# Optimization experiments

Hardware: AMD Instinct MI355X
Metric: run time of the kernel (lower is better)

The kernel has to match this reference:

```python
import jax, jax.numpy as jnp
import numpy as np

B, L = 32, 512
D_EMB = 500      # tagger_mlp_layer
LANG = 100       # tagger_embeddings_size
H = 800          # tagger_encoder_size * 2
P_ARC = 100      # parser_arc_proj_size
P_LAB = 400      # parser_label_proj_size
MLP = 500        # tagger_mlp_layer (aux_mlp out)
N_LANG, N_LAB, N_UPOS, N_XPOS, N_ATTRS = 8, 50, 20, 300, 500


def setup_inputs() -> dict:
    key = jax.random.key(0)
    ks = jax.random.split(key, 24)
    s = 0.05
    lang_table = jax.random.normal(ks[3], (N_LANG, LANG), jnp.float32) * s
    lang_table = lang_table.at[0].set(0.0)  # padding_idx=0
    return {
        "emb": jax.random.normal(ks[0], (B, L, D_EMB), jnp.float32),
        "hidden": jax.random.normal(ks[1], (B, L, H), jnp.float32),
        "lang_ids": jax.random.randint(ks[2], (B,), 0, N_LANG),
        "lang_table": lang_table,
        "W_arc": jax.random.normal(ks[4], (P_ARC, D_EMB + LANG), jnp.float32) * s,
        "b_arc": jax.random.normal(ks[5], (P_ARC,), jnp.float32) * s,
        "W_lab": jax.random.normal(ks[6], (P_LAB, D_EMB + LANG), jnp.float32) * s,
        "b_lab": jax.random.normal(ks[7], (P_LAB,), jnp.float32) * s,
        "w_head": jax.random.normal(ks[8], (2 * P_ARC,), jnp.float32) * s,
        "b_head": jax.random.normal(ks[9], (1,), jnp.float32) * s,
        "W_aux": jax.random.normal(ks[10], (MLP, H), jnp.float32) * s,
        "b_aux": jax.random.normal(ks[11], (MLP,), jnp.float32) * s,
        "W_upos": jax.random.normal(ks[12], (N_UPOS, MLP + LANG), jnp.float32) * s,
        "b_upos": jax.random.normal(ks[13], (N_UPOS,), jnp.float32) * s,
        "W_xpos": jax.random.normal(ks[14], (N_XPOS, MLP + LANG), jnp.float32) * s,
        "b_xpos": jax.random.normal(ks[15], (N_XPOS,), jnp.float32) * s,
        "W_attrs": jax.random.normal(ks[16], (N_ATTRS, MLP + LANG), jnp.float32) * s,
        "b_attrs": jax.random.normal(ks[17], (N_ATTRS,), jnp.float32) * s,
    }


def reference(emb, hidden, lang_ids, lang_table, W_arc, b_arc, W_lab, b_lab,
              w_head, b_head, W_aux, b_aux, W_upos, b_upos, W_xpos, b_xpos,
              W_attrs, b_attrs):
    Bv, Lv = emb.shape[0], emb.shape[1]
    lang_emb = lang_table[lang_ids]                              # [B, LANG]
    lang_rep = jnp.broadcast_to(lang_emb[:, None, :], (Bv, Lv, lang_emb.shape[-1]))
    ho = jnp.concatenate((emb, lang_rep), axis=2)                # [B, L, D_EMB+LANG]

    proj_arc = jnp.tanh(jnp.einsum('bld,pd->blp', ho, W_arc) + b_arc)   # [B, L, P_ARC]
    proj_label = jnp.tanh(jnp.einsum('bld,pd->blp', ho, W_lab) + b_lab) # [B, L, P_LAB]

    # Biaffine decomposition of output_head(cat(pa[i], pa[j])):
    # score(i,j) = pa[i] . w1 + pa[j] . w2 + b
    P = proj_arc.shape[-1]
    s1 = proj_arc @ w_head[:P]                                   # [B, L]
    s2 = proj_arc @ w_head[P:]                                   # [B, L]
    core = s1[:, :, None] + s2[:, None, :] + b_head[0]           # [B, L, L]
    arcs = jnp.concatenate(
        (jnp.zeros((Bv, Lv, 1), core.dtype), core), axis=2)     # [B, L, L+1]

    aux_hid = jnp.tanh(jnp.einsum('blh,mh->blm', hidden, W_aux) + b_aux)  # [B, L, MLP]
    aux_cat = jnp.concatenate((aux_hid, lang_rep), axis=2)
    s_upos = jnp.einsum('blm,um->blu', aux_cat, W_upos) + b_upos
    s_xpos = jnp.einsum('blm,um->blu', aux_cat, W_xpos) + b_xpos
    s_attrs = jnp.einsum('blm,um->blu', aux_cat, W_attrs) + b_attrs
    return arcs, proj_label, s_upos, s_xpos, s_attrs
```

## Files before the change

### kernel.cpp

```cpp
#include <hip/hip_runtime.h>


using f16   = _Float16;
using f16x4 = __attribute__((ext_vector_type(4))) _Float16;
using f16x8 = __attribute__((ext_vector_type(8))) _Float16;
using f32x4 = __attribute__((ext_vector_type(4))) float;

__device__ __forceinline__ f16 f2h(float f) { return (f16)f; }
__device__ __forceinline__ f16x4 cvt4(float4 v) {
  return f16x4{ f2h(v.x), f2h(v.y), f2h(v.z), f2h(v.w) };
}

__device__ __forceinline__ float fast_tanh(float x) {
  float xc = fminf(fmaxf(x, -15.f), 15.f);
  float e  = __builtin_amdgcn_exp2f(xc * 2.885390081777927f);
  return 1.f - 2.f * __builtin_amdgcn_rcpf(e + 1.f);
}

__device__ __forceinline__ void async16(void* lds, const void* gp) {
  __builtin_amdgcn_global_load_lds(
      (const __attribute__((address_space(1))) unsigned int*)gp,
      (__attribute__((address_space(3))) unsigned int*)lds, 16, 0, 0);
}

__global__ __launch_bounds__(256) void setup_kernel(
    const float* __restrict__ emb, const float* __restrict__ hidden,
    const float* __restrict__ lang_table, const int* __restrict__ lang_ids,
    const float* __restrict__ W_arc, const float* __restrict__ b_arc,
    const float* __restrict__ W_lab, const float* __restrict__ b_lab,
    const float* __restrict__ W_aux, const float* __restrict__ b_aux,
    const float* __restrict__ W_upos, const float* __restrict__ b_upos,
    const float* __restrict__ W_xpos, const float* __restrict__ b_xpos,
    const float* __restrict__ W_attrs, const float* __restrict__ b_attrs,
    f16* __restrict__ ho, f16* __restrict__ aux_cat, f16* __restrict__ hid16,
    f16* __restrict__ W_proj, f16* __restrict__ W_auxp, f16* __restrict__ W_heads,
    float* __restrict__ bias_proj, float* __restrict__ bias_aux, float* __restrict__ bias_heads)
{
  const int HID_Q = 16384 * 208;
  const int HO_Q  = 16384 * 160;
  const int W_Q   = 81920 + 106496 + 163840;
  const int TOTAL = HID_Q + HO_Q + W_Q;

  for (int q = blockIdx.x * 256 + threadIdx.x; q < TOTAL; q += gridDim.x * 256) {
    if (q < HID_Q) {
      int row = q / 208, s = q - row * 208;
      f16x4 h = { (f16)0.f, (f16)0.f, (f16)0.f, (f16)0.f };
      if (s < 200) h = cvt4(*(const float4*)(hidden + (size_t)row * 800 + 4 * s));
      *(f16x4*)(hid16 + (size_t)row * 832 + 4 * s) = h;
    } else if (q < HID_Q + HO_Q) {
      int p = q - HID_Q;
      int row = p / 160, s = p - row * 160;
      f16* horow = ho + (size_t)row * 640;
      if (s < 125) {
        float4 v = *(const float4*)(emb + (size_t)row * 500 + 4 * s);
        *(f16x4*)(horow + 4 * s) = cvt4(v);
      } else {
        f16x4 h = { (f16)0.f, (f16)0.f, (f16)0.f, (f16)0.f };
        if (s < 150) {
          const float* lrow = lang_table + (size_t)lang_ids[row >> 9] * 100;
          h = cvt4(*(const float4*)(lrow + (s - 125) * 4));
        }
        *(f16x4*)(horow + 4 * s) = h;
        *(f16x4*)(aux_cat + (size_t)row * 640 + 4 * s) = h;
      }
    } else {
      int w = q - (HID_Q + HO_Q);
      const float* src = nullptr;
      f16* dst;
      if (w < 81920) {
        int n = w / 160, s = w - n * 160;
        dst = W_proj + (size_t)w * 4;
        if (s < 150 && n < 500)
          src = (n < 100 ? W_arc + (size_t)n * 600
                         : W_lab + (size_t)(n - 100) * 600) + s * 4;
      } else if (w < 81920 + 106496) {
        int w2 = w - 81920;
        int n = w2 / 208, s = w2 - n * 208;
        dst = W_auxp + (size_t)w2 * 4;
        if (s < 200 && n < 500) src = W_aux + (size_t)n * 800 + s * 4;
      } else {
        int w3 = w - (81920 + 106496);
        int n = w3 / 160, s = w3 - n * 160;
        dst = W_heads + (size_t)w3 * 4;
        if (s < 150 && n < 820)
          src = (n < 20 ? W_upos + (size_t)n * 600
                : n < 320 ? W_xpos + (size_t)(n - 20) * 600
                          : W_attrs + (size_t)(n - 320) * 600) + s * 4;
      }
      f16x4 h = { (f16)0.f, (f16)0.f, (f16)0.f, (f16)0.f };
      if (src) h = cvt4(*(const float4*)src);
      *(f16x4*)dst = h;
    }
  }

  if (blockIdx.x == 0) {
    for (int idx = threadIdx.x; idx < 2048; idx += 256) {
      if (idx < 512) {
        float v = 0.f;
        if (idx < 100)      v = b_arc[idx];
        else if (idx < 500) v = b_lab[idx - 100];
        bias_proj[idx] = v;
      } else if (idx < 1024) {
        int i = idx - 512;
        bias_aux[i] = (i < 500) ? b_aux[i] : 0.f;
      } else {
        int i = idx - 1024; float v = 0.f;
        if (i < 20)       v = b_upos[i];
        else if (i < 320) v = b_xpos[i - 20];
        else if (i < 820) v = b_attrs[i - 320];
        bias_heads[i] = v;
      }
    }
  }
}

__device__ __forceinline__ void gemm_core256(
    const f16* __restrict__ A, const f16* __restrict__ Bm,
    const int K, const int NT, const int bm, const int bn,
    f16* __restrict__ ldsA, f16* __restrict__ ldsB, f32x4 (&acc)[8][4])
{
  const int tid  = threadIdx.x;
  const int lane = tid & 63;
  const int wave = tid >> 6;
  const int wm = wave >> 2, wn = wave & 3;
  const int m16 = lane & 15, quad = lane >> 4;

  const int sr = lane >> 3;
  const int ss = (lane & 7) ^ sr;
  const f16* gA[4]; const f16* gB[4];
#pragma unroll
  for (int i = 0; i < 4; ++i) {
    gA[i] = A  + (size_t)(bm * 256 + i * 64 + wave * 8 + sr) * K + ss * 8;
    gB[i] = Bm + (size_t)(bn * 256 + i * 64 + wave * 8 + sr) * K + ss * 8;
  }
  f16* sA = ldsA + wave * 512;
  f16* sB = ldsB + wave * 512;

  const int aBase = (wm * 128 + m16) * 64;
  const int bBase = (wn * 64  + m16) * 64;
  const int sw0 = ((quad)     ^ (m16 & 7)) * 8;
  const int sw1 = ((4 | quad) ^ (m16 & 7)) * 8;

  f16x8 af[4], bf[4];

#define RDA(mqv, sw) { _Pragma("unroll")                                        \
  for (int ii = 0; ii < 4; ++ii)                                                \
    af[ii] = *(const f16x8*)&ldsA[buf + aBase + (mqv) * 4096 + ii * 1024 + (sw)]; }
#define RDB(sw) { _Pragma("unroll")                                             \
  for (int j = 0; j < 4; ++j)                                                   \
    bf[j] = *(const f16x8*)&ldsB[buf + bBase + j * 1024 + (sw)]; }
#define MM(mqv) { _Pragma("unroll")                                             \
  for (int ii = 0; ii < 4; ++ii) { _Pragma("unroll")                            \
    for (int j = 0; j < 4; ++j)                                                 \
      acc[(mqv) * 4 + ii][j] = __builtin_amdgcn_mfma_f32_16x16x32_f16(          \
          af[ii], bf[j], acc[(mqv) * 4 + ii][j], 0, 0, 0); } }
#define VM2 { asm volatile("s_waitcnt vmcnt(2)" ::: "memory");                  \
              __builtin_amdgcn_sched_barrier(0); }
#define VM0 { asm volatile("s_waitcnt vmcnt(0)" ::: "memory");                  \
              __builtin_amdgcn_sched_barrier(0); }
#define BAR  __builtin_amdgcn_s_barrier()
#define PRIO1 __builtin_amdgcn_s_setprio(1)
#define PRIO0 __builtin_amdgcn_s_setprio(0)

#pragma unroll
  for (int i = 0; i < 4; ++i) async16(sB + i * 4096, gB[i]);
#pragma unroll
  for (int i = 0; i < 4; ++i) async16(sA + i * 4096, gA[i]);
  VM0;
  BAR;

  for (int t = 0; t < NT; ++t) {
    const int buf = (t & 1) << 14;
    const int nbf = ((t + 1) & 1) << 14;
    const bool st = (t + 1 < NT);
    const int k0n = (t + 1) << 6;

    if (st) { async16(sB + nbf + 0 * 4096, gB[0] + k0n);
              async16(sB + nbf + 1 * 4096, gB[1] + k0n); }
    RDB(sw0); RDA(0, sw0);
    BAR;
    PRIO1; MM(0); PRIO0;
    if (t > 0) { if (st) VM2 else VM0 }
    BAR;
    if (st) { async16(sB + nbf + 2 * 4096, gB[2] + k0n);
              async16(sB + nbf + 3 * 4096, gB[3] + k0n); }
    RDA(1, sw0);
    BAR;
    PRIO1; MM(1); PRIO0;
    BAR;
    if (st) { async16(sA + nbf + 0 * 4096, gA[0] + k0n);
              async16(sA + nbf + 2 * 4096, gA[2] + k0n); }
    RDB(sw1); RDA(0, sw1);
    BAR;
    PRIO1; MM(0); PRIO0;
    BAR;
    if (st) { async16(sA + nbf + 1 * 4096, gA[1] + k0n);
              async16(sA + nbf + 3 * 4096, gA[3] + k0n); }
    RDA(1, sw1);
    BAR;
    PRIO1; MM(1); PRIO0;
    if (st) VM2;
    BAR;
  }
#undef RDA
#undef RDB
#undef MM
#undef VM2
#undef VM0
#undef BAR
#undef PRIO1
#undef PRIO0
}

__global__ __launch_bounds__(512, 2) void gemm01(
    const f16* __restrict__ ho, const f16* __restrict__ hid16,
    const f16* __restrict__ W_proj, const f16* __restrict__ W_auxp,
    const float* __restrict__ bias_proj, const float* __restrict__ bias_aux,
    float* __restrict__ out_label, const float* __restrict__ w_head,
    float* __restrict__ s1, float* __restrict__ s2, f16* __restrict__ aux_cat)
{
  __shared__ __align__(16) f16 ldsA[2 * 16384];
  __shared__ __align__(16) f16 ldsB[2 * 16384];
  __shared__ float s1red[2][256], s2red[2][256];

  const int tid  = threadIdx.x;
  const int lane = tid & 63;
  const int wave = tid >> 6;
  const int wm = wave >> 2, wn = wave & 3;
  const int m16 = lane & 15, quad = lane >> 4;
  const int bm  = blockIdx.x;
  const int bny = blockIdx.y;
  const bool is0 = (bny < 2);
  const int bn  = is0 ? bny : bny - 2;

  const f16* A = is0 ? ho : hid16;
  const f16* B = is0 ? W_proj : W_auxp;
  const float* bias = is0 ? bias_proj : bias_aux;
  const int K  = is0 ? 640 : 832;
  const int NT = is0 ? 10 : 13;

  f32x4 acc[8][4] = {};
  gemm_core256(A, B, K, NT, bm, bn, ldsA, ldsB, acc);

  const int row0 = bm * 256 + wm * 128 + quad * 4;
  const int colT = bn * 256 + wn * 64 + m16;

  if (is0) {
    float p1[8][4] = {}, p2[8][4] = {};
    const bool haveHead = (bn == 0);
#pragma unroll
    for (int ai = 0; ai < 8; ++ai) {
#pragma unroll
      for (int j = 0; j < 4; ++j) {
        const int col = colT + j * 16;
        const float bcol = bias[col];
        float w1c = 0.f, w2c = 0.f;
        if (haveHead && col < 100) { w1c = w_head[col]; w2c = w_head[100 + col]; }
#pragma unroll
        for (int r = 0; r < 4; ++r) {
          const int row = row0 + ai * 16 + r;
          float v = fast_tanh(acc[ai][j][r] + bcol);
          if (col >= 100 && col < 500) out_label[(size_t)row * 400 + col - 100] = v;
          p1[ai][r] += v * w1c;
          p2[ai][r] += v * w2c;
        }
      }
    }
    if (haveHead) {
      if (wn < 2) {
#pragma unroll
        for (int d = 1; d < 16; d <<= 1)
#pragma unroll
          for (int ai = 0; ai < 8; ++ai)
#pragma unroll
            for (int r = 0; r < 4; ++r) {
              p1[ai][r] += __shfl_xor(p1[ai][r], d);
              p2[ai][r] += __shfl_xor(p2[ai][r], d);
            }
        if (m16 == 0) {
#pragma unroll
          for (int ai = 0; ai < 8; ++ai)
#pragma unroll
            for (int r = 0; r < 4; ++r) {
              int rl = wm * 128 + ai * 16 + quad * 4 + r;
              s1red[wn][rl] = p1[ai][r];
              s2red[wn][rl] = p2[ai][r];
            }
        }
      }
      __syncthreads();
      if (tid < 256) s1[bm * 256 + tid] = s1red[0][tid] + s1red[1][tid];
      else { int t2 = tid - 256; s2[bm * 256 + t2] = s2red[0][t2] + s2red[1][t2]; }
    }
  } else {
#pragma unroll
    for (int ai = 0; ai < 8; ++ai)
#pragma unroll
      for (int j = 0; j < 4; ++j) {
        const int col = colT + j * 16;
        if (col < 500) {
          const float bcol = bias[col];
#pragma unroll
          for (int r = 0; r < 4; ++r) {
            const int row = row0 + ai * 16 + r;
            aux_cat[(size_t)row * 640 + col] = f2h(fast_tanh(acc[ai][j][r] + bcol));
          }
        }
      }
  }
}

__global__ __launch_bounds__(512, 2) void gemm2_arcs(
    const f16* __restrict__ aux_cat, const f16* __restrict__ W_heads,
    const float* __restrict__ bias_heads,
    const float* __restrict__ s1, const float* __restrict__ s2,
    const float* __restrict__ b_head,
    float* __restrict__ out_arcs, float* __restrict__ out_upos,
    float* __restrict__ out_xpos, float* __restrict__ out_attrs)
{
  __shared__ __align__(16) f16 ldsA[2 * 16384];
  __shared__ __align__(16) f16 ldsB[2 * 16384];

  const int tid  = threadIdx.x;
  const int lane = tid & 63;
  const int wave = tid >> 6;
  const int wm = wave >> 2, wn = wave & 3;
  const int m16 = lane & 15, quad = lane >> 4;
  const int bm = blockIdx.x, bn = blockIdx.y;

  f32x4 acc[8][4] = {};
  gemm_core256(aux_cat, W_heads, 640, 10, bm, bn, ldsA, ldsB, acc);

  const int row0 = bm * 256 + wm * 128 + quad * 4;
  const int colT = bn * 256 + wn * 64 + m16;
#pragma unroll
  for (int ai = 0; ai < 8; ++ai)
#pragma unroll
    for (int j = 0; j < 4; ++j) {
      const int col = colT + j * 16;
      const float bcol = bias_heads[col];
#pragma unroll
      for (int r = 0; r < 4; ++r) {
        const int row = row0 + ai * 16 + r;
        float v = acc[ai][j][r] + bcol;
        if (col < 20)        out_upos[(size_t)row * 20 + col] = v;
        else if (col < 320)  out_xpos[(size_t)row * 300 + col - 20] = v;
        else if (col < 820)  out_attrs[(size_t)row * 500 + col - 320] = v;
      }
    }

  const int r0 = bm * 256 + bn * 64;
  const float bh = b_head[0];
  const float s2v = s2[((r0 >> 9) << 9) + tid];
  for (int rl = 0; rl < 64; ++rl) {
    const int row = r0 + rl;
    const float s1v = s1[row] + bh;
    float* orow = out_arcs + (size_t)row * 513;
    if (tid == 0) orow[0] = 0.f;
    orow[1 + tid] = s1v + s2v;
  }
}

extern "C" void kernel_launch(void* const* d_in, const int* in_sizes, int n_in,
                              void* d_out, int out_size, void* d_ws, size_t ws_size,
                              hipStream_t stream)
{
  const float* emb      = (const float*)d_in[0];
  const float* hidden   = (const float*)d_in[1];
  const int*   lang_ids = (const int*)d_in[2];
  const float* lang_tab = (const float*)d_in[3];
  const float* W_arc  = (const float*)d_in[4];
  const float* b_arc  = (const float*)d_in[5];
  const float* W_lab  = (const float*)d_in[6];
  const float* b_lab  = (const float*)d_in[7];
  const float* w_head = (const float*)d_in[8];
  const float* b_head = (const float*)d_in[9];
  const float* W_aux  = (const float*)d_in[10];
  const float* b_aux  = (const float*)d_in[11];
  const float* W_upos = (const float*)d_in[12];
  const float* b_upos = (const float*)d_in[13];
  const float* W_xpos = (const float*)d_in[14];
  const float* b_xpos = (const float*)d_in[15];
  const float* W_attrs = (const float*)d_in[16];
  const float* b_attrs = (const float*)d_in[17];

  char* ws = (char*)d_ws;
  f16* ho      = (f16*)(ws + 0);
  f16* aux_cat = (f16*)(ws + 20971520);
  f16* hid16   = (f16*)(ws + 41943040);
  f16* W_proj  = (f16*)(ws + 69206016);
  f16* W_auxp  = (f16*)(ws + 69861376);
  f16* W_heads = (f16*)(ws + 70713344);
  float* bias_proj  = (float*)(ws + 72024064);
  float* bias_aux   = (float*)(ws + 72026112);
  float* bias_heads = (float*)(ws + 72028160);
  float* s1         = (float*)(ws + 72032256);
  float* s2         = (float*)(ws + 72097792);

  float* out       = (float*)d_out;
  float* out_arcs  = out;
  float* out_label = out + 8404992;
  float* out_upos  = out + 14958592;
  float* out_xpos  = out + 15286272;
  float* out_attrs = out + 20201472;

  setup_kernel<<<2048, 256, 0, stream>>>(
      emb, hidden, lang_tab, lang_ids,
      W_arc, b_arc, W_lab, b_lab, W_aux, b_aux,
      W_upos, b_upos, W_xpos, b_xpos, W_attrs, b_attrs,
      ho, aux_cat, hid16, W_proj, W_auxp, W_heads,
      bias_proj, bias_aux, bias_heads);

  gemm01<<<dim3(64, 4), 512, 0, stream>>>(
      ho, hid16, W_proj, W_auxp, bias_proj, bias_aux,
      out_label, w_head, s1, s2, aux_cat);

  gemm2_arcs<<<dim3(64, 4), 512, 0, stream>>>(
      aux_cat, W_heads, bias_heads, s1, s2, b_head,
      out_arcs, out_upos, out_xpos, out_attrs);
}
```

Baseline: 299.0 us.

## Fuse fp32-to-fp16 activation conversion into the first GEMM's A-tile loads

```diff
diff --git a/kernel.cpp b/kernel.cpp
--- a/kernel.cpp
+++ b/kernel.cpp
@@ -24,123 +24,323 @@
 }
 
 __global__ __launch_bounds__(256) void setup_kernel(
-    const float* __restrict__ emb, const float* __restrict__ hidden,
-    const float* __restrict__ lang_table, const int* __restrict__ lang_ids,
     const float* __restrict__ W_arc, const float* __restrict__ b_arc,
     const float* __restrict__ W_lab, const float* __restrict__ b_lab,
     const float* __restrict__ W_aux, const float* __restrict__ b_aux,
     const float* __restrict__ W_upos, const float* __restrict__ b_upos,
     const float* __restrict__ W_xpos, const float* __restrict__ b_xpos,
     const float* __restrict__ W_attrs, const float* __restrict__ b_attrs,
-    f16* __restrict__ ho, f16* __restrict__ aux_cat, f16* __restrict__ hid16,
     f16* __restrict__ W_proj, f16* __restrict__ W_auxp, f16* __restrict__ W_heads,
     float* __restrict__ bias_proj, float* __restrict__ bias_aux, float* __restrict__ bias_heads)
 {
-  const int HID_Q = 16384 * 208;
-  const int HO_Q  = 16384 * 160;
-  const int W_Q   = 81920 + 106496 + 163840;
-  const int TOTAL = HID_Q + HO_Q + W_Q;
-
-  for (int q = blockIdx.x * 256 + threadIdx.x; q < TOTAL; q += gridDim.x * 256) {
-    if (q < HID_Q) {
-      int row = q / 208, s = q - row * 208;
-      f16x4 h = { (f16)0.f, (f16)0.f, (f16)0.f, (f16)0.f };
-      if (s < 200) h = cvt4(*(const float4*)(hidden + (size_t)row * 800 + 4 * s));
-      *(f16x4*)(hid16 + (size_t)row * 832 + 4 * s) = h;
-    } else if (q < HID_Q + HO_Q) {
-      int p = q - HID_Q;
-      int row = p / 160, s = p - row * 160;
-      f16* horow = ho + (size_t)row * 640;
-      if (s < 125) {
-        float4 v = *(const float4*)(emb + (size_t)row * 500 + 4 * s);
-        *(f16x4*)(horow + 4 * s) = cvt4(v);
-      } else {
-        f16x4 h = { (f16)0.f, (f16)0.f, (f16)0.f, (f16)0.f };
-        if (s < 150) {
-          const float* lrow = lang_table + (size_t)lang_ids[row >> 9] * 100;
-          h = cvt4(*(const float4*)(lrow + (s - 125) * 4));
-        }
-        *(f16x4*)(horow + 4 * s) = h;
-        *(f16x4*)(aux_cat + (size_t)row * 640 + 4 * s) = h;
-      }
+  const int blk = blockIdx.x, t = threadIdx.x;
+  if (blk < 1376) {
+    int w = blk * 256 + t;
+    const float* src = nullptr;
+    f16* dst;
+    if (w < 81920) {
+      int n = w / 160, s = w - n * 160;
+      dst = W_proj + (size_t)w * 4;
+      if (s < 150 && n < 500)
+        src = (n < 100 ? W_arc + (size_t)n * 600
+                       : W_lab + (size_t)(n - 100) * 600) + s * 4;
+    } else if (w < 81920 + 106496) {
+      int w2 = w - 81920;
+      int n = w2 / 208, s = w2 - n * 208;
+      dst = W_auxp + (size_t)w2 * 4;
+      if (s < 200 && n < 500) src = W_aux + (size_t)n * 800 + s * 4;
     } else {
-      int w = q - (HID_Q + HO_Q);
-      const float* src = nullptr;
-      f16* dst;
-      if (w < 81920) {
-        int n = w / 160, s = w - n * 160;
-        dst = W_proj + (size_t)w * 4;
-        if (s < 150 && n < 500)
-          src = (n < 100 ? W_arc + (size_t)n * 600
-                         : W_lab + (size_t)(n - 100) * 600) + s * 4;
-      } else if (w < 81920 + 106496) {
-        int w2 = w - 81920;
-        int n = w2 / 208, s = w2 - n * 208;
-        dst = W_auxp + (size_t)w2 * 4;
-        if (s < 200 && n < 500) src = W_aux + (size_t)n * 800 + s * 4;
-      } else {
-        int w3 = w - (81920 + 106496);
-        int n = w3 / 160, s = w3 - n * 160;
-        dst = W_heads + (size_t)w3 * 4;
-        if (s < 150 && n < 820)
-          src = (n < 20 ? W_upos + (size_t)n * 600
-                : n < 320 ? W_xpos + (size_t)(n - 20) * 600
-                          : W_attrs + (size_t)(n - 320) * 600) + s * 4;
-      }
-      f16x4 h = { (f16)0.f, (f16)0.f, (f16)0.f, (f16)0.f };
-      if (src) h = cvt4(*(const float4*)src);
-      *(f16x4*)dst = h;
-    }
-  }
-
-  if (blockIdx.x == 0) {
-    for (int idx = threadIdx.x; idx < 2048; idx += 256) {
-      if (idx < 512) {
-        float v = 0.f;
-        if (idx < 100)      v = b_arc[idx];
-        else if (idx < 500) v = b_lab[idx - 100];
-        bias_proj[idx] = v;
-      } else if (idx < 1024) {
-        int i = idx - 512;
-        bias_aux[i] = (i < 500) ? b_aux[i] : 0.f;
-      } else {
-        int i = idx - 1024; float v = 0.f;
-        if (i < 20)       v = b_upos[i];
-        else if (i < 320) v = b_xpos[i - 20];
-        else if (i < 820) v = b_attrs[i - 320];
-        bias_heads[i] = v;
-      }
-    }
-  }
-}
-
-__device__ __forceinline__ void gemm_core256(
-    const f16* __restrict__ A, const f16* __restrict__ Bm,
-    const int K, const int NT, const int bm, const int bn,
-    f16* __restrict__ ldsA, f16* __restrict__ ldsB, f32x4 (&acc)[8][4])
+      int w3 = w - (81920 + 106496);
+      int n = w3 / 160, s = w3 - n * 160;
+      dst = W_heads + (size_t)w3 * 4;
+      if (s < 150 && n < 820)
+        src = (n < 20 ? W_upos + (size_t)n * 600
+              : n < 320 ? W_xpos + (size_t)(n - 20) * 600
+                        : W_attrs + (size_t)(n - 320) * 600) + s * 4;
+    }
+    f16x4 h = { (f16)0.f, (f16)0.f, (f16)0.f, (f16)0.f };
+    if (src) h = cvt4(*(const float4*)src);
+    *(f16x4*)dst = h;
+    return;
+  }
+  for (int idx = t; idx < 2048; idx += 256) {
+    if (idx < 512) {
+      float v = 0.f;
+      if (idx < 100)      v = b_arc[idx];
+      else if (idx < 500) v = b_lab[idx - 100];
+      bias_proj[idx] = v;
+    } else if (idx < 1024) {
+      int i = idx - 512;
+      bias_aux[i] = (i < 500) ? b_aux[i] : 0.f;
+    } else {
+      int i = idx - 1024; float v = 0.f;
+      if (i < 20)       v = b_upos[i];
+      else if (i < 320) v = b_xpos[i - 20];
+      else if (i < 820) v = b_attrs[i - 320];
+      bias_heads[i] = v;
+    }
+  }
+}
+
+__global__ __launch_bounds__(512, 2) void gemm01(
+    const float* __restrict__ emb, const float* __restrict__ hidden,
+    const float* __restrict__ lang_table, const int* __restrict__ lang_ids,
+    const f16* __restrict__ W_proj, const f16* __restrict__ W_auxp,
+    const float* __restrict__ bias_proj, const float* __restrict__ bias_aux,
+    float* __restrict__ out_label, const float* __restrict__ w_head,
+    float* __restrict__ s1, float* __restrict__ s2, f16* __restrict__ aux_cat)
 {
+  __shared__ __align__(16) f16 ldsA[2 * 16384];
+  __shared__ __align__(16) f16 ldsB[2 * 16384];
+  __shared__ float s1red[2][256], s2red[2][256];
+
   const int tid  = threadIdx.x;
   const int lane = tid & 63;
   const int wave = tid >> 6;
   const int wm = wave >> 2, wn = wave & 3;
   const int m16 = lane & 15, quad = lane >> 4;
+  const int bm  = blockIdx.x;
+  const int bny = blockIdx.y;
+  const bool is0 = (bny < 2);
+  const int bn  = is0 ? bny : bny - 2;
+  const int K   = is0 ? 640 : 832;
+  const int NT  = is0 ? 10 : 13;
 
   const int sr = lane >> 3;
-  const int ss = (lane & 7) ^ sr;
-  const f16* gA[4]; const f16* gB[4];
+  const int ssB = (lane & 7) ^ sr;
+  const f16* Bmat = is0 ? W_proj : W_auxp;
+  const f16* gB[4];
+#pragma unroll
+  for (int i = 0; i < 4; ++i)
+    gB[i] = Bmat + (size_t)(bn * 256 + i * 64 + wave * 8 + sr) * K + ssB * 8;
+  f16* sB = ldsB + wave * 512;
+
+  const int ssA = lane & 7;
+  const float* lrow = lang_table + (size_t)lang_ids[bm >> 1] * 100;
+  const float* srcA[4];
+  int dstA[4];
 #pragma unroll
   for (int i = 0; i < 4; ++i) {
-    gA[i] = A  + (size_t)(bm * 256 + i * 64 + wave * 8 + sr) * K + ss * 8;
-    gB[i] = Bm + (size_t)(bn * 256 + i * 64 + wave * 8 + sr) * K + ss * 8;
-  }
-  f16* sA = ldsA + wave * 512;
-  f16* sB = ldsB + wave * 512;
+    const int rowA = wave * 32 + i * 8 + (lane >> 3);
+    const int grow = bm * 256 + rowA;
+    srcA[i] = is0 ? emb + (size_t)grow * 500 : hidden + (size_t)grow * 800;
+    dstA[i] = rowA * 64 + ((ssA ^ (rowA & 7)) * 8);
+  }
+  float4 va[4], vb[4];
 
   const int aBase = (wm * 128 + m16) * 64;
   const int bBase = (wn * 64  + m16) * 64;
   const int sw0 = ((quad)     ^ (m16 & 7)) * 8;
   const int sw1 = ((4 | quad) ^ (m16 & 7)) * 8;
 
+  f32x4 acc[8][4] = {};
+  f16x8 af[4], bf[4];
+
+#define ASTAGE(tt) do { const int k0b = (tt) * 64 + ssA * 8;                    \
+    _Pragma("unroll")                                                           \
+    for (int i2 = 0; i2 < 4; ++i2) {                                            \
+      float4 x0 = {0.f,0.f,0.f,0.f}, x1 = {0.f,0.f,0.f,0.f};                    \
+      if (is0) {                                                                \
+        if (k0b < 500) { x0 = *(const float4*)(srcA[i2] + k0b);                 \
+          x1 = (k0b + 4 < 500) ? *(const float4*)(srcA[i2] + k0b + 4)           \
+                               : *(const float4*)(lrow); }                      \
+        else if (k0b < 600) { x0 = *(const float4*)(lrow + k0b - 500);          \
+                              x1 = *(const float4*)(lrow + k0b - 496); }        \
+      } else if (k0b < 800) { x0 = *(const float4*)(srcA[i2] + k0b);            \
+                              x1 = *(const float4*)(srcA[i2] + k0b + 4); }      \
+      va[i2] = x0; vb[i2] = x1; } } while (0)
+
+#define AWRITE(nbf) do { _Pragma("unroll")                                      \
+    for (int i2 = 0; i2 < 4; ++i2) {                                            \
+      f16x8 hw = { f2h(va[i2].x), f2h(va[i2].y), f2h(va[i2].z), f2h(va[i2].w),  \
+                   f2h(vb[i2].x), f2h(vb[i2].y), f2h(vb[i2].z), f2h(vb[i2].w) };\
+      *(f16x8*)&ldsA[(nbf) + dstA[i2]] = hw; } } while (0)
+
+#define RDA(mqv, sw) { _Pragma("unroll")                                        \
+  for (int ii = 0; ii < 4; ++ii)                                                \
+    af[ii] = *(const f16x8*)&ldsA[buf + aBase + (mqv) * 4096 + ii * 1024 + (sw)]; }
+#define RDB(sw) { _Pragma("unroll")                                             \
+  for (int j = 0; j < 4; ++j)                                                   \
+    bf[j] = *(const f16x8*)&ldsB[buf + bBase + j * 1024 + (sw)]; }
+#define MM(mqv) { _Pragma("unroll")                                             \
+  for (int ii = 0; ii < 4; ++ii) { _Pragma("unroll")                            \
+    for (int j = 0; j < 4; ++j)                                                 \
+      acc[(mqv) * 4 + ii][j] = __builtin_amdgcn_mfma_f32_16x16x32_f16(          \
+          af[ii], bf[j], acc[(mqv) * 4 + ii][j], 0, 0, 0); } }
+#define VM0 { asm volatile("s_waitcnt vmcnt(0)" ::: "memory");                  \
+              __builtin_amdgcn_sched_barrier(0); }
+#define LGK0 { asm volatile("s_waitcnt lgkmcnt(0)" ::: "memory");               \
+               __builtin_amdgcn_sched_barrier(0); }
+#define BAR  __builtin_amdgcn_s_barrier()
+#define PRIO1 __builtin_amdgcn_s_setprio(1)
+#define PRIO0 __builtin_amdgcn_s_setprio(0)
+
+#pragma unroll
+  for (int i = 0; i < 4; ++i) async16(sB + i * 4096, gB[i]);
+  ASTAGE(0);
+  VM0;
+  AWRITE(0);
+  LGK0;
+  BAR;
+
+  for (int t = 0; t < NT; ++t) {
+    const int buf = (t & 1) << 14;
+    const int nbf = ((t + 1) & 1) << 14;
+    const bool st = (t + 1 < NT);
+    const int k0n = (t + 1) << 6;
+
+    if (st) {
+      async16(sB + nbf + 0 * 4096, gB[0] + k0n);
+      async16(sB + nbf + 1 * 4096, gB[1] + k0n);
+      async16(sB + nbf + 2 * 4096, gB[2] + k0n);
+      async16(sB + nbf + 3 * 4096, gB[3] + k0n);
+      ASTAGE(t + 1);
+    }
+    RDB(sw0); RDA(0, sw0);
+    BAR;
+    PRIO1; MM(0); PRIO0;
+    BAR;
+    RDA(1, sw0);
+    BAR;
+    PRIO1; MM(1); PRIO0;
+    BAR;
+    RDB(sw1); RDA(0, sw1);
+    BAR;
+    PRIO1; MM(0); PRIO0;
+    BAR;
+    RDA(1, sw1);
+    if (st) { VM0; AWRITE(nbf); }
+    LGK0;
+    BAR;
+    PRIO1; MM(1); PRIO0;
+    BAR;
+  }
+#undef ASTAGE
+#undef AWRITE
+#undef RDA
+#undef RDB
+#undef MM
+#undef VM0
+#undef LGK0
+#undef BAR
+#undef PRIO1
+#undef PRIO0
+
+  const int row0 = bm * 256 + wm * 128 + quad * 4;
+  const int colT = bn * 256 + wn * 64 + m16;
+
+  if (is0) {
+    const float* bias = bias_proj;
+    float p1[8][4] = {}, p2[8][4] = {};
+    const bool haveHead = (bn == 0);
+#pragma unroll
+    for (int ai = 0; ai < 8; ++ai) {
+#pragma unroll
+      for (int j = 0; j < 4; ++j) {
+        const int col = colT + j * 16;
+        const float bcol = bias[col];
+        float w1c = 0.f, w2c = 0.f;
+        if (haveHead && col < 100) { w1c = w_head[col]; w2c = w_head[100 + col]; }
+#pragma unroll
+        for (int r = 0; r < 4; ++r) {
+          const int row = row0 + ai * 16 + r;
+          float v = fast_tanh(acc[ai][j][r] + bcol);
+          if (col >= 100 && col < 500) out_label[(size_t)row * 400 + col - 100] = v;
+          p1[ai][r] += v * w1c;
+          p2[ai][r] += v * w2c;
+        }
+      }
+    }
+    if (haveHead) {
+      if (wn < 2) {
+#pragma unroll
+        for (int d = 1; d < 16; d <<= 1)
+#pragma unroll
+          for (int ai = 0; ai < 8; ++ai)
+#pragma unroll
+            for (int r = 0; r < 4; ++r) {
+              p1[ai][r] += __shfl_xor(p1[ai][r], d);
+              p2[ai][r] += __shfl_xor(p2[ai][r], d);
+            }
+        if (m16 == 0) {
+#pragma unroll
+          for (int ai = 0; ai < 8; ++ai)
+#pragma unroll
+            for (int r = 0; r < 4; ++r) {
+              int rl = wm * 128 + ai * 16 + quad * 4 + r;
+              s1red[wn][rl] = p1[ai][r];
+              s2red[wn][rl] = p2[ai][r];
+            }
+        }
+      }
+      __syncthreads();
+      if (tid < 256) s1[bm * 256 + tid] = s1red[0][tid] + s1red[1][tid];
+      else { int t2 = tid - 256; s2[bm * 256 + t2] = s2red[0][t2] + s2red[1][t2]; }
+    }
+  } else {
+    const float* bias = bias_aux;
+#pragma unroll
+    for (int ai = 0; ai < 8; ++ai)
+#pragma unroll
+      for (int j = 0; j < 4; ++j) {
+        const int col = colT + j * 16;
+        if (col < 500) {
+          const float bcol = bias[col];
+#pragma unroll
+          for (int r = 0; r < 4; ++r) {
+            const int row = row0 + ai * 16 + r;
+            aux_cat[(size_t)row * 640 + col] = f2h(fast_tanh(acc[ai][j][r] + bcol));
+          }
+        }
+      }
+    if (bn == 0) {
+      for (int idx = tid; idx < 256 * 35; idx += 512) {
+        int rr = idx / 35, qq = idx - rr * 35;
+        int col = 500 + 4 * qq;
+        f16x4 h = { (f16)0.f, (f16)0.f, (f16)0.f, (f16)0.f };
+        if (col < 600) h = cvt4(*(const float4*)(lrow + col - 500));
+        *(f16x4*)(aux_cat + (size_t)(bm * 256 + rr) * 640 + col) = h;
+      }
+    }
+  }
+}
+
+__global__ __launch_bounds__(512, 2) void gemm2_arcs(
+    const f16* __restrict__ aux_cat, const f16* __restrict__ W_heads,
+    const float* __restrict__ bias_heads,
+    const float* __restrict__ s1, const float* __restrict__ s2,
+    const float* __restrict__ b_head,
+    float* __restrict__ out_arcs, float* __restrict__ out_upos,
+    float* __restrict__ out_xpos, float* __restrict__ out_attrs)
+{
+  __shared__ __align__(16) f16 ldsA[2 * 16384];
+  __shared__ __align__(16) f16 ldsB[2 * 16384];
+
+  const int tid  = threadIdx.x;
+  const int lane = tid & 63;
+  const int wave = tid >> 6;
+  const int wm = wave >> 2, wn = wave & 3;
+  const int m16 = lane & 15, quad = lane >> 4;
+  const int bm = blockIdx.x, bn = blockIdx.y;
+  const int K = 640, NT = 10;
+
+  const int sr = lane >> 3;
+  const int ss = (lane & 7) ^ sr;
+  const f16* gA[4]; const f16* gB[4];
+#pragma unroll
+  for (int i = 0; i < 4; ++i) {
+    gA[i] = aux_cat + (size_t)(bm * 256 + i * 64 + wave * 8 + sr) * K + ss * 8;
+    gB[i] = W_heads + (size_t)(bn * 256 + i * 64 + wave * 8 + sr) * K + ss * 8;
+  }
+  f16* sA = ldsA + wave * 512;
+  f16* sB = ldsB + wave * 512;
+
+  const int aBase = (wm * 128 + m16) * 64;
+  const int bBase = (wn * 64  + m16) * 64;
+  const int sw0 = ((quad)     ^ (m16 & 7)) * 8;
+  const int sw1 = ((4 | quad) ^ (m16 & 7)) * 8;
+
+  f32x4 acc[8][4] = {};
   f16x8 af[4], bf[4];
 
 #define RDA(mqv, sw) { _Pragma("unroll")                                        \
@@ -210,126 +410,6 @@
 #undef BAR
 #undef PRIO1
 #undef PRIO0
-}
-
-__global__ __launch_bounds__(512, 2) void gemm01(
-    const f16* __restrict__ ho, const f16* __restrict__ hid16,
-    const f16* __restrict__ W_proj, const f16* __restrict__ W_auxp,
-    const float* __restrict__ bias_proj, const float* __restrict__ bias_aux,
-    float* __restrict__ out_label, const float* __restrict__ w_head,
-    float* __restrict__ s1, float* __restrict__ s2, f16* __restrict__ aux_cat)
-{
-  __shared__ __align__(16) f16 ldsA[2 * 16384];
-  __shared__ __align__(16) f16 ldsB[2 * 16384];
-  __shared__ float s1red[2][256], s2red[2][256];
-
-  const int tid  = threadIdx.x;
-  const int lane = tid & 63;
-  const int wave = tid >> 6;
-  const int wm = wave >> 2, wn = wave & 3;
-  const int m16 = lane & 15, quad = lane >> 4;
-  const int bm  = blockIdx.x;
-  const int bny = blockIdx.y;
-  const bool is0 = (bny < 2);
-  const int bn  = is0 ? bny : bny - 2;
-
-  const f16* A = is0 ? ho : hid16;
-  const f16* B = is0 ? W_proj : W_auxp;
-  const float* bias = is0 ? bias_proj : bias_aux;
-  const int K  = is0 ? 640 : 832;
-  const int NT = is0 ? 10 : 13;
-
-  f32x4 acc[8][4] = {};
-  gemm_core256(A, B, K, NT, bm, bn, ldsA, ldsB, acc);
-
-  const int row0 = bm * 256 + wm * 128 + quad * 4;
-  const int colT = bn * 256 + wn * 64 + m16;
-
-  if (is0) {
-    float p1[8][4] = {}, p2[8][4] = {};
-    const bool haveHead = (bn == 0);
-#pragma unroll
-    for (int ai = 0; ai < 8; ++ai) {
-#pragma unroll
-      for (int j = 0; j < 4; ++j) {
-        const int col = colT + j * 16;
-        const float bcol = bias[col];
-        float w1c = 0.f, w2c = 0.f;
-        if (haveHead && col < 100) { w1c = w_head[col]; w2c = w_head[100 + col]; }
-#pragma unroll
-        for (int r = 0; r < 4; ++r) {
-          const int row = row0 + ai * 16 + r;
-          float v = fast_tanh(acc[ai][j][r] + bcol);
-          if (col >= 100 && col < 500) out_label[(size_t)row * 400 + col - 100] = v;
-          p1[ai][r] += v * w1c;
-          p2[ai][r] += v * w2c;
-        }
-      }
-    }
-    if (haveHead) {
-      if (wn < 2) {
-#pragma unroll
-        for (int d = 1; d < 16; d <<= 1)
-#pragma unroll
-          for (int ai = 0; ai < 8; ++ai)
-#pragma unroll
-            for (int r = 0; r < 4; ++r) {
-              p1[ai][r] += __shfl_xor(p1[ai][r], d);
-              p2[ai][r] += __shfl_xor(p2[ai][r], d);
-            }
-        if (m16 == 0) {
-#pragma unroll
-          for (int ai = 0; ai < 8; ++ai)
-#pragma unroll
-            for (int r = 0; r < 4; ++r) {
-              int rl = wm * 128 + ai * 16 + quad * 4 + r;
-              s1red[wn][rl] = p1[ai][r];
-              s2red[wn][rl] = p2[ai][r];
-            }
-        }
-      }
-      __syncthreads();
-      if (tid < 256) s1[bm * 256 + tid] = s1red[0][tid] + s1red[1][tid];
-      else { int t2 = tid - 256; s2[bm * 256 + t2] = s2red[0][t2] + s2red[1][t2]; }
-    }
-  } else {
-#pragma unroll
-    for (int ai = 0; ai < 8; ++ai)
-#pragma unroll
-      for (int j = 0; j < 4; ++j) {
-        const int col = colT + j * 16;
-        if (col < 500) {
-          const float bcol = bias[col];
-#pragma unroll
-          for (int r = 0; r < 4; ++r) {
-            const int row = row0 + ai * 16 + r;
-            aux_cat[(size_t)row * 640 + col] = f2h(fast_tanh(acc[ai][j][r] + bcol));
-          }
-        }
-      }
-  }
-}
-
-__global__ __launch_bounds__(512, 2) void gemm2_arcs(
-    const f16* __restrict__ aux_cat, const f16* __restrict__ W_heads,
-    const float* __restrict__ bias_heads,
-    const float* __restrict__ s1, const float* __restrict__ s2,
-    const float* __restrict__ b_head,
-    float* __restrict__ out_arcs, float* __restrict__ out_upos,
-    float* __restrict__ out_xpos, float* __restrict__ out_attrs)
-{
-  __shared__ __align__(16) f16 ldsA[2 * 16384];
-  __shared__ __align__(16) f16 ldsB[2 * 16384];
-
-  const int tid  = threadIdx.x;
-  const int lane = tid & 63;
-  const int wave = tid >> 6;
-  const int wm = wave >> 2, wn = wave & 3;
-  const int m16 = lane & 15, quad = lane >> 4;
-  const int bm = blockIdx.x, bn = blockIdx.y;
-
-  f32x4 acc[8][4] = {};
-  gemm_core256(aux_cat, W_heads, 640, 10, bm, bn, ldsA, ldsB, acc);
 
   const int row0 = bm * 256 + wm * 128 + quad * 4;
   const int colT = bn * 256 + wn * 64 + m16;
@@ -385,17 +465,15 @@
   const float* b_attrs = (const float*)d_in[17];
 
   char* ws = (char*)d_ws;
-  f16* ho      = (f16*)(ws + 0);
-  f16* aux_cat = (f16*)(ws + 20971520);
-  f16* hid16   = (f16*)(ws + 41943040);
-  f16* W_proj  = (f16*)(ws + 69206016);
-  f16* W_auxp  = (f16*)(ws + 69861376);
-  f16* W_heads = (f16*)(ws + 70713344);
-  float* bias_proj  = (float*)(ws + 72024064);
-  float* bias_aux   = (float*)(ws + 72026112);
-  float* bias_heads = (float*)(ws + 72028160);
-  float* s1         = (float*)(ws + 72032256);
-  float* s2         = (float*)(ws + 72097792);
+  f16* aux_cat = (f16*)(ws + 0);
+  f16* W_proj  = (f16*)(ws + 20971520);
+  f16* W_auxp  = (f16*)(ws + 21626880);
+  f16* W_heads = (f16*)(ws + 22478848);
+  float* bias_proj  = (float*)(ws + 23789568);
+  float* bias_aux   = (float*)(ws + 23791616);
+  float* bias_heads = (float*)(ws + 23793664);
+  float* s1         = (float*)(ws + 23797760);
+  float* s2         = (float*)(ws + 23863296);
 
   float* out       = (float*)d_out;
   float* out_arcs  = out;
@@ -404,15 +482,13 @@
   float* out_xpos  = out + 15286272;
   float* out_attrs = out + 20201472;
 
-  setup_kernel<<<2048, 256, 0, stream>>>(
-      emb, hidden, lang_tab, lang_ids,
+  setup_kernel<<<1377, 256, 0, stream>>>(
       W_arc, b_arc, W_lab, b_lab, W_aux, b_aux,
       W_upos, b_upos, W_xpos, b_xpos, W_attrs, b_attrs,
-      ho, aux_cat, hid16, W_proj, W_auxp, W_heads,
-      bias_proj, bias_aux, bias_heads);
+      W_proj, W_auxp, W_heads, bias_proj, bias_aux, bias_heads);
 
   gemm01<<<dim3(64, 4), 512, 0, stream>>>(
-      ho, hid16, W_proj, W_auxp, bias_proj, bias_aux,
+      emb, hidden, lang_tab, lang_ids, W_proj, W_auxp, bias_proj, bias_aux,
       out_label, w_head, s1, s2, aux_cat);
 
   gemm2_arcs<<<dim3(64, 4), 512, 0, stream>>>(
```

Result: faster. 283.4 us (-5.2%).
